# Kernel tuning notes

Measured on AMD Instinct MI355X. Metric: run time of the kernel, lower is better.

Reference implementation:

```python
import jax, jax.numpy as jnp
import numpy as np


def gcn_conv(x, src, dst, W, b, N):
    """PyG GCNConv: add self-loops, symmetric D^-1/2 (A+I) D^-1/2 normalization."""
    loop = jnp.arange(N, dtype=src.dtype)
    s = jnp.concatenate([src, loop])
    d = jnp.concatenate([dst, loop])
    deg = jnp.zeros((N,), dtype=x.dtype).at[d].add(1.0)  # in-degree incl. self-loop
    dinv = jax.lax.rsqrt(deg)  # deg >= 1 because of self-loops
    norm = dinv[s] * dinv[d]  # [E+N]
    h = x @ W  # [N, out] linear transform first (as in PyG)
    msg = h[s] * norm[:, None]  # gather + scale
    out = jax.ops.segment_sum(msg, d, num_segments=N)  # scatter-add
    return out + b


def setup_inputs() -> dict:
    key = jax.random.key(0)
    ks = jax.random.split(key, 10)
    N, E, in_dim, h1, h2, A = 100000, 3200000, 256, 32, 64, 64
    x = jax.random.normal(ks[0], (N, in_dim), dtype=jnp.float32)
    ei = jax.random.randint(ks[1], (2, E), 0, N, dtype=jnp.int64)
    def glorot(k, shape):
        lim = float(np.sqrt(6.0 / (shape[0] + shape[1])))
        return jax.random.uniform(k, shape, jnp.float32, -lim, lim)
    return {
        "x": x,
        "ei": ei,
        "num_nodes": N,
        "W1": glorot(ks[2], (in_dim, h1)), "b1": jnp.zeros((h1,), jnp.float32),
        "W2": glorot(ks[3], (h1, h2)),     "b2": jnp.zeros((h2,), jnp.float32),
        "Wo1": glorot(ks[4], (h2, h2)),    "bo1": jnp.zeros((h2,), jnp.float32),
        "Wo2": glorot(ks[5], (h2, A)),     "bo2": jnp.zeros((A,), jnp.float32),
    }


def reference(x, ei, num_nodes, W1, b1, W2, b2, Wo1, bo1, Wo2, bo2):
    src, dst = ei[0], ei[1]
    z = jax.nn.relu(gcn_conv(x, src, dst, W1, b1, num_nodes))
    z = jax.nn.relu(gcn_conv(z, src, dst, W2, b2, num_nodes))
    logits = jax.nn.relu(z @ Wo1 + bo1) @ Wo2 + bo2  # [N, action_space]
    nbatches = z.shape[0] // num_nodes
    # original reshapes with z.size(1)=hidden2 (== action_space here)
    dist = logits.reshape(nbatches, num_nodes * z.shape[1])
    return jax.nn.softmax(dist, axis=-1)  # Categorical probs
```

## Files before the change

### kernel.cpp

```cpp
#include <hip/hip_runtime.h>

#define DEVI __device__ __forceinline__

DEVI unsigned fkey(float f) {
  unsigned u = __float_as_uint(f);
  return u ^ ((u >> 31) ? 0xFFFFFFFFu : 0x80000000u);
}
DEVI float funkey(unsigned k) {
  unsigned b = (k & 0x80000000u) ? (k ^ 0x80000000u) : ~k;
  return __uint_as_float(b);
}
DEVI float f4get(const float4& v, int j) {
  return j == 0 ? v.x : j == 1 ? v.y : j == 2 ? v.z : v.w;
}

constexpr int BSH = 9;
constexpr int BNODES = 1 << BSH;
constexpr int PEPT = 16;
constexpr int PCHUNK = 256 * PEPT;

__global__ void k_binit(int* __restrict__ bcnt) {
  bcnt[threadIdx.x] = 0;
}

__global__ void k_bcount(const int* __restrict__ dst, int* __restrict__ bcnt,
                         int E, int NB) {
  __shared__ int lh[256];
  lh[threadIdx.x] = 0;
  __syncthreads();
  int stride = gridDim.x * 256;
  for (long i = (long)blockIdx.x * 256 + threadIdx.x; i < E; i += stride)
    atomicAdd(&lh[dst[i] >> BSH], 1);
  __syncthreads();
  if (threadIdx.x < NB && lh[threadIdx.x]) atomicAdd(&bcnt[threadIdx.x], lh[threadIdx.x]);
}

__global__ void k_bscan(const int* __restrict__ bcnt, int* __restrict__ bbase,
                        int* __restrict__ bcur, unsigned* __restrict__ scal, int NB) {
  __shared__ int s[256];
  int t = threadIdx.x;
  int v = (t < NB) ? bcnt[t] : 0;
  s[t] = v;
  __syncthreads();
  for (int o = 1; o < 256; o <<= 1) {
    int add = (t >= o) ? s[t - o] : 0;
    __syncthreads();
    s[t] += add;
    __syncthreads();
  }
  int excl = s[t] - v;
  if (t < NB) { bbase[t] = excl; bcur[t] = excl; }
  if (t == 0) { scal[0] = 0u; scal[1] = 0u; }
}

__global__ __launch_bounds__(256)
void k_bpart(const int* __restrict__ src, const int* __restrict__ dst,
             int* __restrict__ bcur, unsigned* __restrict__ epart, int E, int NB) {
  __shared__ int lh[256];
  __shared__ int gbase[256];
  long base = (long)blockIdx.x * PCHUNK;
  lh[threadIdx.x] = 0;
  __syncthreads();
  int ed[PEPT]; int es[PEPT]; unsigned short lpos[PEPT];
#pragma unroll
  for (int j = 0; j < PEPT; j++) {
    long i = base + threadIdx.x + (long)j * 256;
    if (i < E) {
      int d = dst[i];
      es[j] = src[i];
      ed[j] = d;
      lpos[j] = (unsigned short)atomicAdd(&lh[d >> BSH], 1);
    } else {
      ed[j] = -1;
    }
  }
  __syncthreads();
  if (threadIdx.x < NB) {
    int c = lh[threadIdx.x];
    gbase[threadIdx.x] = c ? atomicAdd(&bcur[threadIdx.x], c) : 0;
  }
  __syncthreads();
#pragma unroll
  for (int j = 0; j < PEPT; j++) {
    int d = ed[j];
    if (d >= 0) {
      unsigned p = (unsigned)(gbase[d >> BSH] + (int)lpos[j]);
      epart[p] = ((unsigned)(d & (BNODES - 1)) << 17) | (unsigned)es[j];
    }
  }
}

__global__ __launch_bounds__(256)
void k_fine(const unsigned* __restrict__ epart, const int* __restrict__ bbase,
            const int* __restrict__ bcnt, int* __restrict__ rowptr,
            int* __restrict__ deg, float* __restrict__ dinv,
            int* __restrict__ col, int N) {
  __shared__ int lh[BNODES];
  __shared__ int lexcl[BNODES];
  __shared__ int ssc[256];
  int b = blockIdx.x;
  int base = bbase[b], cnt = bcnt[b];
  int nlo = b << BSH;
  int t = threadIdx.x;
  lh[t] = 0; lh[t + 256] = 0;
  __syncthreads();
  for (int i = t; i < cnt; i += 256) {
    unsigned e = epart[base + i];
    atomicAdd(&lh[e >> 17], 1);
  }
  __syncthreads();
  int a0 = lh[2 * t], a1 = lh[2 * t + 1];
  ssc[t] = a0 + a1;
  __syncthreads();
  for (int o = 1; o < 256; o <<= 1) {
    int add = (t >= o) ? ssc[t - o] : 0;
    __syncthreads();
    ssc[t] += add;
    __syncthreads();
  }
  int excl = ssc[t] - (a0 + a1);
  lexcl[2 * t] = excl;
  lexcl[2 * t + 1] = excl + a0;
  __syncthreads();
#pragma unroll
  for (int k = 0; k < 2; k++) {
    int i = t + k * 256;
    int v = nlo + i;
    if (v < N) {
      int dgv = lh[i];
      deg[v] = dgv;
      rowptr[v] = base + lexcl[i];
      dinv[v] = rsqrtf((float)(dgv + 1));
    }
  }
  __syncthreads();
  lh[2 * t] = lexcl[2 * t];
  lh[2 * t + 1] = lexcl[2 * t + 1];
  __syncthreads();
  for (int i = t; i < cnt; i += 256) {
    unsigned e = epart[base + i];
    int p = atomicAdd(&lh[e >> 17], 1);
    col[base + p] = (int)(e & 0x1FFFFu);
  }
}

__global__ __launch_bounds__(512)
void k_gemm1(const float* __restrict__ in, const float* __restrict__ W,
             const float* __restrict__ dinv, float* __restrict__ out, int N) {
  __shared__ float Wl[256 * 32];
  __shared__ float red[256 * 8];
  int t = threadIdx.x;
  int kh = t >> 8;
  int tl = t & 255;
  int cg = tl & 3, rg = tl >> 2;
  int c0 = cg * 8;
  long r0 = (long)blockIdx.x * 64 + rg;
  bool rv = r0 < (long)N;

  for (int i = t; i < 256 * 32; i += 512) Wl[i] = W[i];
  __syncthreads();

  const float* ip = in + r0 * 256 + kh * 128;
  const float* wp = &Wl[kh * 128 * 32];

  float acc[8];
#pragma unroll
  for (int c = 0; c < 8; c++) acc[c] = 0.f;

#pragma unroll 2
  for (int k = 0; k < 128; k += 4) {
    float4 xv = rv ? *(const float4*)(ip + k) : make_float4(0.f, 0.f, 0.f, 0.f);
#pragma unroll
    for (int jj = 0; jj < 4; jj++) {
      const float4 wa = *(const float4*)&wp[(k + jj) * 32 + c0];
      const float4 wb = *(const float4*)&wp[(k + jj) * 32 + c0 + 4];
      float xs = f4get(xv, jj);
      acc[0] = fmaf(xs, wa.x, acc[0]);
      acc[1] = fmaf(xs, wa.y, acc[1]);
      acc[2] = fmaf(xs, wa.z, acc[2]);
      acc[3] = fmaf(xs, wa.w, acc[3]);
      acc[4] = fmaf(xs, wb.x, acc[4]);
      acc[5] = fmaf(xs, wb.y, acc[5]);
      acc[6] = fmaf(xs, wb.z, acc[6]);
      acc[7] = fmaf(xs, wb.w, acc[7]);
    }
  }

  if (kh) {
    float* rp = &red[tl * 8];
    *(float4*)(rp) = make_float4(acc[0], acc[1], acc[2], acc[3]);
    *(float4*)(rp + 4) = make_float4(acc[4], acc[5], acc[6], acc[7]);
  }
  __syncthreads();
  if (!kh && rv) {
    const float* rp = &red[tl * 8];
    float4 ha = *(const float4*)(rp);
    float4 hb = *(const float4*)(rp + 4);
    float dv = dinv[r0];
    float* op = &out[r0 * 32 + c0];
    *(float4*)(op) = make_float4((acc[0] + ha.x) * dv, (acc[1] + ha.y) * dv,
                                 (acc[2] + ha.z) * dv, (acc[3] + ha.w) * dv);
    *(float4*)(op + 4) = make_float4((acc[4] + hb.x) * dv, (acc[5] + hb.y) * dv,
                                     (acc[6] + hb.z) * dv, (acc[7] + hb.w) * dv);
  }
}

template <int K, int COLS, int ROWS, bool BIAS, bool RELU, bool SCALE, bool DOMAX>
__launch_bounds__(256)
__global__ void k_gemm(const float* __restrict__ in, const float* __restrict__ W,
                       const float* __restrict__ bias, const float* __restrict__ dinv,
                       float* __restrict__ out, int N, unsigned* __restrict__ gmax) {
  constexpr int CG = COLS / 8;
  constexpr int RG = 256 / CG;
  constexpr int RPB = RG * ROWS;
  __shared__ float Wl[K * COLS];
  for (int i = threadIdx.x; i < K * COLS; i += 256) Wl[i] = W[i];
  __syncthreads();

  int cg = threadIdx.x % CG, rg = threadIdx.x / CG;
  int c0 = cg * 8;
  long r0 = (long)blockIdx.x * RPB + rg * ROWS;

  float acc[ROWS][8];
#pragma unroll
  for (int i = 0; i < ROWS; i++)
#pragma unroll
    for (int c = 0; c < 8; c++) acc[i][c] = 0.f;
  bool rv[ROWS];
#pragma unroll
  for (int i = 0; i < ROWS; i++) rv[i] = (r0 + i) < (long)N;

  const float* ip = in + r0 * K;
#pragma unroll 2
  for (int k = 0; k < K; k += 4) {
    float4 xv[ROWS];
#pragma unroll
    for (int i = 0; i < ROWS; i++)
      xv[i] = rv[i] ? *(const float4*)(ip + (long)i * K + k) : make_float4(0.f, 0.f, 0.f, 0.f);
#pragma unroll
    for (int jj = 0; jj < 4; jj++) {
      const float4 wa = *(const float4*)&Wl[(k + jj) * COLS + c0];
      const float4 wb = *(const float4*)&Wl[(k + jj) * COLS + c0 + 4];
#pragma unroll
      for (int i = 0; i < ROWS; i++) {
        float xs = f4get(xv[i], jj);
        acc[i][0] = fmaf(xs, wa.x, acc[i][0]);
        acc[i][1] = fmaf(xs, wa.y, acc[i][1]);
        acc[i][2] = fmaf(xs, wa.z, acc[i][2]);
        acc[i][3] = fmaf(xs, wa.w, acc[i][3]);
        acc[i][4] = fmaf(xs, wb.x, acc[i][4]);
        acc[i][5] = fmaf(xs, wb.y, acc[i][5]);
        acc[i][6] = fmaf(xs, wb.z, acc[i][6]);
        acc[i][7] = fmaf(xs, wb.w, acc[i][7]);
      }
    }
  }

  float bo[8];
  if (BIAS) {
#pragma unroll
    for (int c = 0; c < 8; c++) bo[c] = bias[c0 + c];
  }
  float m = -3.4e38f;
#pragma unroll
  for (int i = 0; i < ROWS; i++) {
    if (!rv[i]) continue;
    float dv = SCALE ? dinv[r0 + i] : 1.f;
    float o[8];
#pragma unroll
    for (int c = 0; c < 8; c++) {
      float v = acc[i][c];
      if (BIAS) v += bo[c];
      if (SCALE) v *= dv;
      if (RELU) v = fmaxf(v, 0.f);
      if (DOMAX) m = fmaxf(m, v);
      o[c] = v;
    }
    float* op = &out[(r0 + i) * COLS + c0];
    *(float4*)(op) = make_float4(o[0], o[1], o[2], o[3]);
    *(float4*)(op + 4) = make_float4(o[4], o[5], o[6], o[7]);
  }
  if constexpr (DOMAX) {
    __shared__ float red[256];
    red[threadIdx.x] = m;
    __syncthreads();
    for (int o = 128; o > 0; o >>= 1) {
      if (threadIdx.x < o) red[threadIdx.x] = fmaxf(red[threadIdx.x], red[threadIdx.x + o]);
      __syncthreads();
    }
    if (threadIdx.x == 0) atomicMax(gmax, fkey(red[0]));
  }
}

template <int FEAT, bool BIAS, bool RELU, bool PSCALE>
__launch_bounds__(256)
__global__ void k_aggv(const float* __restrict__ g, const int* __restrict__ col,
                       const int* __restrict__ rowptr, const int* __restrict__ deg,
                       const float* __restrict__ dinv, const float* __restrict__ bias,
                       float* __restrict__ out, int N) {
  constexpr int LPN = FEAT / 4;
  constexpr int NPB = 256 / LPN;
  int nib = threadIdx.x / LPN;
  int c = threadIdx.x % LPN;
  long v = (long)blockIdx.x * NPB + nib;
  if (v >= N) return;

  const float4* g4 = (const float4*)g;
  float4 acc = g4[v * LPN + c];
  int start = rowptr[v], dg = deg[v];
  int e = 0;
  while (e < dg) {
    int cnt = min(LPN, dg - e);
    int idx = (c < cnt) ? col[start + e + c] : 0;
    int j = 0;
    for (; j + 4 <= cnt; j += 4) {
      int u0 = __shfl(idx, j + 0, LPN);
      int u1 = __shfl(idx, j + 1, LPN);
      int u2 = __shfl(idx, j + 2, LPN);
      int u3 = __shfl(idx, j + 3, LPN);
      float4 a0 = g4[(long)u0 * LPN + c];
      float4 a1 = g4[(long)u1 * LPN + c];
      float4 a2 = g4[(long)u2 * LPN + c];
      float4 a3 = g4[(long)u3 * LPN + c];
      acc.x += (a0.x + a1.x) + (a2.x + a3.x);
      acc.y += (a0.y + a1.y) + (a2.y + a3.y);
      acc.z += (a0.z + a1.z) + (a2.z + a3.z);
      acc.w += (a0.w + a1.w) + (a2.w + a3.w);
    }
    for (; j < cnt; j++) {
      int u = __shfl(idx, j, LPN);
      float4 a = g4[(long)u * LPN + c];
      acc.x += a.x; acc.y += a.y; acc.z += a.z; acc.w += a.w;
    }
    e += cnt;
  }
  float dv = dinv[v];
  float4 val;
  val.x = acc.x * dv; val.y = acc.y * dv; val.z = acc.z * dv; val.w = acc.w * dv;
  if (BIAS) {
    float4 b = ((const float4*)bias)[c];
    val.x += b.x; val.y += b.y; val.z += b.z; val.w += b.w;
  }
  if (RELU) {
    val.x = fmaxf(val.x, 0.f); val.y = fmaxf(val.y, 0.f);
    val.z = fmaxf(val.z, 0.f); val.w = fmaxf(val.w, 0.f);
  }
  if (PSCALE) {
    val.x *= dv; val.y *= dv; val.z *= dv; val.w *= dv;
  }
  ((float4*)out)[v * LPN + c] = val;
}

__global__ void k_smsum(const float* __restrict__ logit, unsigned* __restrict__ scal, int total) {
  __shared__ float s[256];
  float gmax = funkey(scal[0]);
  float loc = 0.f;
  for (int i = blockIdx.x * 256 + threadIdx.x; i < total; i += gridDim.x * 256)
    loc += expf(logit[i] - gmax);
  s[threadIdx.x] = loc; __syncthreads();
  for (int o = 128; o > 0; o >>= 1) {
    if (threadIdx.x < o) s[threadIdx.x] += s[threadIdx.x + o];
    __syncthreads();
  }
  if (threadIdx.x == 0) atomicAdd((float*)&scal[1], s[0]);
}

__global__ void k_smnorm(float* __restrict__ logit, const unsigned* __restrict__ scal, int total) {
  float gmax = funkey(scal[0]);
  float inv = 1.0f / __uint_as_float(scal[1]);
  int i = blockIdx.x * 256 + threadIdx.x;
  if (i < total) logit[i] = expf(logit[i] - gmax) * inv;
}

extern "C" void kernel_launch(void* const* d_in, const int* in_sizes, int n_in,
                              void* d_out, int out_size, void* d_ws, size_t ws_size,
                              hipStream_t stream) {
  const float* x   = (const float*)d_in[0];
  const int*   ei  = (const int*)d_in[1];
  const float* W1  = (const float*)d_in[3];
  const float* b1  = (const float*)d_in[4];
  const float* W2  = (const float*)d_in[5];
  const float* b2  = (const float*)d_in[6];
  const float* Wo1 = (const float*)d_in[7];
  const float* bo1 = (const float*)d_in[8];
  const float* Wo2 = (const float*)d_in[9];
  const float* bo2 = (const float*)d_in[10];

  const int N = in_sizes[0] / 256;
  const int E = in_sizes[1] / 2;
  const int* src = ei;
  const int* dst = ei + E;
  const int NB = (N + BNODES - 1) / BNODES;

  size_t o = 0;
  auto carve = [&](size_t bytes) -> char* {
    char* p = (char*)d_ws + o;
    o += (bytes + 255) & ~(size_t)255;
    return p;
  };
  float* R1     = (float*)carve((size_t)N * 64 * 4);
  float* R2     = (float*)carve((size_t)N * 64 * 4);
  int*   col    = (int*)carve((size_t)E * 4);
  int*   deg    = (int*)carve((size_t)N * 4);
  float* dinv   = (float*)carve((size_t)N * 4);
  int*   rowptr = (int*)carve((size_t)N * 4);
  int*   bcnt   = (int*)carve(256 * 4);
  int*   bbase  = (int*)carve(256 * 4);
  int*   bcur   = (int*)carve(256 * 4);
  unsigned* scal = (unsigned*)carve(64);

  unsigned* epart = (unsigned*)R2;
  float* g1 = R1;
  float* p  = R2;
  float* s2 = R1;
  float* z2 = R2;
  float* t  = R1;
  float* logits = (float*)d_out;

  k_binit<<<1, 256, 0, stream>>>(bcnt);
  k_bcount<<<512, 256, 0, stream>>>(dst, bcnt, E, NB);
  k_bscan<<<1, 256, 0, stream>>>(bcnt, bbase, bcur, scal, NB);
  k_bpart<<<(E + PCHUNK - 1) / PCHUNK, 256, 0, stream>>>(src, dst, bcur, epart, E, NB);
  k_fine<<<NB, 256, 0, stream>>>(epart, bbase, bcnt, rowptr, deg, dinv, col, N);

  const int gG = (N + 63) / 64;
  const int gA = (N + 31) / 32;

  k_gemm1<<<gG, 512, 0, stream>>>(x, W1, dinv, g1, N);
  k_aggv<32, true, true, true><<<gA, 256, 0, stream>>>(g1, col, rowptr, deg, dinv, b1, p, N);

  k_aggv<32, false, false, false><<<gA, 256, 0, stream>>>(p, col, rowptr, deg, dinv, nullptr, s2, N);
  k_gemm<32, 64, 2, true, true, false, false>
      <<<gG, 256, 0, stream>>>(s2, W2, b2, nullptr, z2, N, nullptr);

  k_gemm<64, 64, 2, true, true, false, false>
      <<<gG, 256, 0, stream>>>(z2, Wo1, bo1, nullptr, t, N, nullptr);
  k_gemm<64, 64, 2, true, false, false, true>
      <<<gG, 256, 0, stream>>>(t, Wo2, bo2, nullptr, logits, N, scal);

  k_smsum<<<1024, 256, 0, stream>>>(logits, scal, out_size);
  k_smnorm<<<(out_size + 255) / 256, 256, 0, stream>>>(logits, scal, out_size);
}
```

Before: 538.9 us.

## Restructure first GEMM to wave-uniform weight loads without LDS or split-K

The first-layer GEMM (x @ W1) is rewritten so that each wave owns one 8-column group and each lane owns one row. The weight index is made wave-uniform with readfirstlane, so W1 can be read through scalar loads instead of being staged in LDS. This removes the LDS fill, the split-K halves, the shared-memory reduction and both block barriers, and drops the block from 512 to 256 threads. The cost is that each lane now strides 1 KB across rows when reading x, and each row of x is read by four separate waves. Coalescing and cache reuse of the input matrix may therefore suffer.

Result: slower. 553.6 us (+2.7%).

```diff
diff --git a/kernel.cpp b/kernel.cpp
--- a/kernel.cpp
+++ b/kernel.cpp
@@ -144,64 +144,45 @@
   }
 }
 
-__global__ __launch_bounds__(512)
+__global__ __launch_bounds__(256)
 void k_gemm1(const float* __restrict__ in, const float* __restrict__ W,
              const float* __restrict__ dinv, float* __restrict__ out, int N) {
-  __shared__ float Wl[256 * 32];
-  __shared__ float red[256 * 8];
   int t = threadIdx.x;
-  int kh = t >> 8;
-  int tl = t & 255;
-  int cg = tl & 3, rg = tl >> 2;
-  int c0 = cg * 8;
-  long r0 = (long)blockIdx.x * 64 + rg;
-  bool rv = r0 < (long)N;
-
-  for (int i = t; i < 256 * 32; i += 512) Wl[i] = W[i];
-  __syncthreads();
-
-  const float* ip = in + r0 * 256 + kh * 128;
-  const float* wp = &Wl[kh * 128 * 32];
+  int lane = t & 63;
+  int c0 = __builtin_amdgcn_readfirstlane((t >> 6) * 8);
+  long r = (long)blockIdx.x * 64 + lane;
+  bool rv = r < (long)N;
+
+  const float* ip = in + r * 256;
+  const float* wp = W + c0;
 
   float acc[8];
 #pragma unroll
   for (int c = 0; c < 8; c++) acc[c] = 0.f;
 
 #pragma unroll 2
-  for (int k = 0; k < 128; k += 4) {
+  for (int k = 0; k < 256; k += 4) {
     float4 xv = rv ? *(const float4*)(ip + k) : make_float4(0.f, 0.f, 0.f, 0.f);
 #pragma unroll
     for (int jj = 0; jj < 4; jj++) {
-      const float4 wa = *(const float4*)&wp[(k + jj) * 32 + c0];
-      const float4 wb = *(const float4*)&wp[(k + jj) * 32 + c0 + 4];
+      const float* wr = wp + (k + jj) * 32;
       float xs = f4get(xv, jj);
-      acc[0] = fmaf(xs, wa.x, acc[0]);
-      acc[1] = fmaf(xs, wa.y, acc[1]);
-      acc[2] = fmaf(xs, wa.z, acc[2]);
-      acc[3] = fmaf(xs, wa.w, acc[3]);
-      acc[4] = fmaf(xs, wb.x, acc[4]);
-      acc[5] = fmaf(xs, wb.y, acc[5]);
-      acc[6] = fmaf(xs, wb.z, acc[6]);
-      acc[7] = fmaf(xs, wb.w, acc[7]);
-    }
-  }
-
-  if (kh) {
-    float* rp = &red[tl * 8];
-    *(float4*)(rp) = make_float4(acc[0], acc[1], acc[2], acc[3]);
-    *(float4*)(rp + 4) = make_float4(acc[4], acc[5], acc[6], acc[7]);
-  }
-  __syncthreads();
-  if (!kh && rv) {
-    const float* rp = &red[tl * 8];
-    float4 ha = *(const float4*)(rp);
-    float4 hb = *(const float4*)(rp + 4);
-    float dv = dinv[r0];
-    float* op = &out[r0 * 32 + c0];
-    *(float4*)(op) = make_float4((acc[0] + ha.x) * dv, (acc[1] + ha.y) * dv,
-                                 (acc[2] + ha.z) * dv, (acc[3] + ha.w) * dv);
-    *(float4*)(op + 4) = make_float4((acc[4] + hb.x) * dv, (acc[5] + hb.y) * dv,
-                                     (acc[6] + hb.z) * dv, (acc[7] + hb.w) * dv);
+      acc[0] = fmaf(xs, wr[0], acc[0]);
+      acc[1] = fmaf(xs, wr[1], acc[1]);
+      acc[2] = fmaf(xs, wr[2], acc[2]);
+      acc[3] = fmaf(xs, wr[3], acc[3]);
+      acc[4] = fmaf(xs, wr[4], acc[4]);
+      acc[5] = fmaf(xs, wr[5], acc[5]);
+      acc[6] = fmaf(xs, wr[6], acc[6]);
+      acc[7] = fmaf(xs, wr[7], acc[7]);
+    }
+  }
+
+  if (rv) {
+    float dv = dinv[r];
+    float* op = &out[r * 32 + c0];
+    *(float4*)(op) = make_float4(acc[0] * dv, acc[1] * dv, acc[2] * dv, acc[3] * dv);
+    *(float4*)(op + 4) = make_float4(acc[4] * dv, acc[5] * dv, acc[6] * dv, acc[7] * dv);
   }
 }
 
@@ -426,7 +407,7 @@
   const int gG = (N + 63) / 64;
   const int gA = (N + 31) / 32;
 
-  k_gemm1<<<gG, 512, 0, stream>>>(x, W1, dinv, g1, N);
+  k_gemm1<<<gG, 256, 0, stream>>>(x, W1, dinv, g1, N);
   k_aggv<32, true, true, true><<<gA, 256, 0, stream>>>(g1, col, rowptr, deg, dinv, b1, p, N);
 
   k_aggv<32, false, false, false><<<gA, 256, 0, stream>>>(p, col, rowptr, deg, dinv, nullptr, s2, N);
```
